# Kernel tuning notes

Hardware: AMD Instinct MI355X
Metric: run time of the kernel (lower is better)

Reference implementation:

```python
import jax, jax.numpy as jnp
import numpy as np

OUT_H, OUT_W = 7, 7
SCALE = 0.25
S = 2  # sample_num per bin axis


def _bilinear(img, y, x):
    """Bilinearly sample img[..., H, W] at float coords (y, x).
    y, x have identical shape G; returns img.shape[:-2] + G.
    Matches RoIAlign CUDA interpolation (zero outside [-1, H]/[-1, W])."""
    H, W = img.shape[-2], img.shape[-1]
    valid = (y > -1.0) & (y < H) & (x > -1.0) & (x < W)
    y = jnp.clip(y, 0.0, H - 1)
    x = jnp.clip(x, 0.0, W - 1)
    y0 = jnp.floor(y).astype(jnp.int32)
    x0 = jnp.floor(x).astype(jnp.int32)
    y1 = jnp.minimum(y0 + 1, H - 1)
    x1 = jnp.minimum(x0 + 1, W - 1)
    ly = y - y0
    lx = x - x0
    hy, hx = 1.0 - ly, 1.0 - lx
    v = (hy * hx * img[..., y0, x0] + hy * lx * img[..., y0, x1]
         + ly * hx * img[..., y1, x0] + ly * lx * img[..., y1, x1])
    return jnp.where(valid, v, 0.0)


def setup_inputs() -> dict:
    key = jax.random.key(0)
    k1, k2, k3, k4, k5 = jax.random.split(key, 5)
    N, C, H, W = 2, 256, 200, 200
    R, MH, MW = 512, 128, 128
    features = jax.random.normal(k1, (N, C, H, W), jnp.float32)
    bidx = jax.random.randint(k2, (R,), 0, N)
    xy1 = jax.random.randint(k3, (R, 2), 0, 672)          # x1, y1 (image coords)
    wh = jax.random.randint(k4, (R, 2), 8, 128)           # box sizes in [8,128)
    xy2 = jnp.minimum(xy1 + wh - 1, 799)                  # x2, y2 inclusive
    rois = jnp.concatenate([bidx[:, None].astype(jnp.float32),
                            xy1.astype(jnp.float32),
                            xy2.astype(jnp.float32)], axis=1)  # [R,5]
    batch_masks = jax.random.uniform(k5, (R, MH, MW), jnp.float32)
    # zero-pad beyond each roi's (h, w), mimicking the list->dense packing
    hv = jnp.arange(MH)[None, :] < (xy2[:, 1] - xy1[:, 1] + 1)[:, None]
    wv = jnp.arange(MW)[None, :] < (xy2[:, 0] - xy1[:, 0] + 1)[:, None]
    batch_masks = batch_masks * (hv[:, :, None] & wv[:, None, :]).astype(jnp.float32)
    return {"features": features, "rois": rois, "batch_masks": batch_masks}


def reference(features, rois, batch_masks):
    """Mask-weighted RoIAlign: per-roi bilinear feature samples are weighted by
    the roi's shape mask (bilinearly sampled in roi-relative image coords),
    then average-pooled over the sub-sample grid of each output bin."""
    C = features.shape[1]

    def one_roi(roi, mask):
        b = roi[0].astype(jnp.int32)
        x1, y1, x2, y2 = roi[1], roi[2], roi[3], roi[4]
        roi_start_w = x1 * SCALE
        roi_start_h = y1 * SCALE
        roi_w = jnp.maximum((x2 - x1 + 1.0) * SCALE, 1.0)
        roi_h = jnp.maximum((y2 - y1 + 1.0) * SCALE, 1.0)
        bin_w = roi_w / OUT_W
        bin_h = roi_h / OUT_H
        # sub-sample offsets: (bin + (i+0.5)/S) for i in [0,S)  -> [OUT*S]
        offs = (jnp.arange(S, dtype=jnp.float32) + 0.5) / S
        ys = roi_start_h + (jnp.arange(OUT_H, dtype=jnp.float32)[:, None] + offs[None, :]).reshape(-1) * bin_h
        xs = roi_start_w + (jnp.arange(OUT_W, dtype=jnp.float32)[:, None] + offs[None, :]).reshape(-1) * bin_w
        yy, xx = jnp.meshgrid(ys, xs, indexing='ij')       # [OUT_H*S, OUT_W*S]
        feat = features[b]                                  # [C, H, W]
        vals = _bilinear(feat, yy, xx)                      # [C, OUT_H*S, OUT_W*S]
        # mask weight at the same sample point, in roi-relative image coords
        my = jnp.clip(yy / SCALE - y1, 0.0, y2 - y1)
        mx = jnp.clip(xx / SCALE - x1, 0.0, x2 - x1)
        wgt = _bilinear(mask, my, mx)                       # [OUT_H*S, OUT_W*S]
        v = (vals * wgt).reshape(C, OUT_H, S, OUT_W, S)
        return v.mean(axis=(2, 4))                          # [C, OUT_H, OUT_W]

    return jax.vmap(one_roi)(rois, batch_masks)             # [R, C, OUT_H, OUT_W]
```

## Files before the change

kernel.cpp:

```cpp
#include <hip/hip_runtime.h>


constexpr int   OUT_H = 7, OUT_W = 7;
constexpr int   NBIN  = OUT_H * OUT_W;
constexpr float SCALE = 0.25f;
constexpr int   S     = 2;
constexpr int   NSAMP = NBIN * S * S;

__global__ __launch_bounds__(256)
void nchw_to_nhwc_kernel(const float* __restrict__ in, float* __restrict__ out,
                         int C, int P) {
    __shared__ float tile[32][33];
    int tx = threadIdx.x;
    int ty = threadIdx.y;
    int gx = blockIdx.x * 32;
    int gy = blockIdx.y * 32;
    int b  = blockIdx.z;

    const float* inb  = in  + (size_t)b * C * P;
    float*       outb = out + (size_t)b * C * P;

#pragma unroll
    for (int j = 0; j < 4; ++j) {
        int cc = gy + ty + 8 * j;
        int p  = gx + tx;
        if (cc < C && p < P)
            tile[ty + 8 * j][tx] = inb[(size_t)cc * P + p];
    }
    __syncthreads();
#pragma unroll
    for (int j = 0; j < 4; ++j) {
        int p  = gx + ty + 8 * j;
        int cc = gy + tx;
        if (cc < C && p < P)
            outb[(size_t)p * C + cc] = tile[tx][ty + 8 * j];
    }
}

__global__ __launch_bounds__(256)
void mask_roialign_nhwc_kernel(const float* __restrict__ nhwc,
                               const float* __restrict__ rois,
                               const float* __restrict__ masks,
                               float*       __restrict__ out,
                               int C, int H, int W, int MH, int MW) {
    __shared__ int   s_off[NSAMP][4];
    __shared__ float s_w[NSAMP][4];
    __shared__ float s_out[256 * NBIN];

    const int r   = blockIdx.x;
    const int tid = threadIdx.x;

    const float* roi = rois + (size_t)r * 5;
    const int   b  = (int)roi[0];
    const float x1 = roi[1], y1 = roi[2], x2 = roi[3], y2 = roi[4];

    if (tid < NSAMP) {
        const int bin = tid >> 2;
        const int sub = tid & 3;
        const int ph  = bin / OUT_W, pw = bin % OUT_W;
        const int iy  = sub >> 1,   ix = sub & 1;

        const float roi_start_w = x1 * SCALE;
        const float roi_start_h = y1 * SCALE;
        const float roi_w = fmaxf((x2 - x1 + 1.0f) * SCALE, 1.0f);
        const float roi_h = fmaxf((y2 - y1 + 1.0f) * SCALE, 1.0f);
        const float bin_w = roi_w / (float)OUT_W;
        const float bin_h = roi_h / (float)OUT_H;

        const float yy = roi_start_h + ((float)ph + ((float)iy + 0.5f) * (1.0f / S)) * bin_h;
        const float xx = roi_start_w + ((float)pw + ((float)ix + 0.5f) * (1.0f / S)) * bin_w;

        const bool valid = (yy > -1.0f) && (yy < (float)H) && (xx > -1.0f) && (xx < (float)W);

        const float* msk = masks + (size_t)r * MH * MW;
        float my = fminf(fmaxf(yy * (1.0f / SCALE) - y1, 0.0f), y2 - y1);
        float mx = fminf(fmaxf(xx * (1.0f / SCALE) - x1, 0.0f), x2 - x1);
        {
            my = fminf(fmaxf(my, 0.0f), (float)(MH - 1));
            mx = fminf(fmaxf(mx, 0.0f), (float)(MW - 1));
        }
        const int my0 = (int)floorf(my), mx0 = (int)floorf(mx);
        const int my1 = min(my0 + 1, MH - 1), mx1 = min(mx0 + 1, MW - 1);
        const float mly = my - (float)my0, mlx = mx - (float)mx0;
        const float mhy = 1.0f - mly,      mhx = 1.0f - mlx;
        const float wgt = mhy * mhx * msk[my0 * MW + mx0] + mhy * mlx * msk[my0 * MW + mx1]
                        + mly * mhx * msk[my1 * MW + mx0] + mly * mlx * msk[my1 * MW + mx1];

        const float yc = fminf(fmaxf(yy, 0.0f), (float)(H - 1));
        const float xc = fminf(fmaxf(xx, 0.0f), (float)(W - 1));
        const int y0  = (int)floorf(yc), x0 = (int)floorf(xc);
        const int y1i = min(y0 + 1, H - 1), x1i = min(x0 + 1, W - 1);
        const float ly = yc - (float)y0, lx = xc - (float)x0;
        const float hy = 1.0f - ly,      hx = 1.0f - lx;

        const float scale_all = (valid ? wgt : 0.0f) * (1.0f / (float)(S * S));
        s_w[tid][0] = hy * hx * scale_all;
        s_w[tid][1] = hy * lx * scale_all;
        s_w[tid][2] = ly * hx * scale_all;
        s_w[tid][3] = ly * lx * scale_all;
        s_off[tid][0] = (y0  * W + x0 ) * C;
        s_off[tid][1] = (y0  * W + x1i) * C;
        s_off[tid][2] = (y1i * W + x0 ) * C;
        s_off[tid][3] = (y1i * W + x1i) * C;
    }
    __syncthreads();

    const int c = tid;
    const float* f = nhwc + (size_t)b * H * W * C + c;

    for (int bin = 0; bin < NBIN; ++bin) {
        float acc = 0.0f;
#pragma unroll
        for (int sub = 0; sub < 4; ++sub) {
            const int s = bin * 4 + sub;
            const int   o0 = s_off[s][0], o1 = s_off[s][1], o2 = s_off[s][2], o3 = s_off[s][3];
            const float w0 = s_w[s][0],   w1 = s_w[s][1],   w2 = s_w[s][2],   w3 = s_w[s][3];
            acc += w0 * f[o0] + w1 * f[o1] + w2 * f[o2] + w3 * f[o3];
        }
        s_out[c * NBIN + bin] = acc;
    }
    __syncthreads();

    float* outr = out + (size_t)r * C * NBIN;
    const float4* s4 = (const float4*)s_out;
    float4*       o4 = (float4*)outr;
    const int nvec = (256 * NBIN) / 4;
    for (int i = tid; i < nvec; i += 256)
        o4[i] = s4[i];
}

__global__ __launch_bounds__(256)
void mask_roialign_kernel(const float* __restrict__ features,
                          const float* __restrict__ rois,
                          const float* __restrict__ masks,
                          float*       __restrict__ out,
                          int C, int H, int W, int MH, int MW) {
    int blk = blockIdx.x;
    int pw  = blk % OUT_W;
    int ph  = (blk / OUT_W) % OUT_H;
    int r   = blk / (OUT_W * OUT_H);
    int c   = threadIdx.x;

    const float* roi = rois + (size_t)r * 5;
    int   b  = (int)roi[0];
    float x1 = roi[1], y1 = roi[2], x2 = roi[3], y2 = roi[4];

    float roi_start_w = x1 * SCALE;
    float roi_start_h = y1 * SCALE;
    float roi_w = fmaxf((x2 - x1 + 1.0f) * SCALE, 1.0f);
    float roi_h = fmaxf((y2 - y1 + 1.0f) * SCALE, 1.0f);
    float bin_w = roi_w / (float)OUT_W;
    float bin_h = roi_h / (float)OUT_H;

    const float* fch = features + ((size_t)b * C + c) * (size_t)(H * W);
    const float* msk = masks + (size_t)r * MH * MW;

    float acc = 0.0f;
#pragma unroll
    for (int iy = 0; iy < S; ++iy) {
        float yy = roi_start_h + ((float)ph + ((float)iy + 0.5f) / (float)S) * bin_h;
#pragma unroll
        for (int ix = 0; ix < S; ++ix) {
            float xx = roi_start_w + ((float)pw + ((float)ix + 0.5f) / (float)S) * bin_w;
            bool valid = (yy > -1.0f) && (yy < (float)H) && (xx > -1.0f) && (xx < (float)W);
            float my = fminf(fmaxf(yy / SCALE - y1, 0.0f), fminf(y2 - y1, (float)(MH - 1)));
            float mx = fminf(fmaxf(xx / SCALE - x1, 0.0f), fminf(x2 - x1, (float)(MW - 1)));
            int my0 = (int)floorf(my), mx0 = (int)floorf(mx);
            int my1 = min(my0 + 1, MH - 1), mx1 = min(mx0 + 1, MW - 1);
            float mly = my - my0, mlx = mx - mx0, mhy = 1.0f - mly, mhx = 1.0f - mlx;
            float wgt = mhy * mhx * msk[my0 * MW + mx0] + mhy * mlx * msk[my0 * MW + mx1]
                      + mly * mhx * msk[my1 * MW + mx0] + mly * mlx * msk[my1 * MW + mx1];
            if (valid) {
                float yc = fminf(fmaxf(yy, 0.0f), (float)(H - 1));
                float xc = fminf(fmaxf(xx, 0.0f), (float)(W - 1));
                int y0 = (int)floorf(yc), x0 = (int)floorf(xc);
                int y1i = min(y0 + 1, H - 1), x1i = min(x0 + 1, W - 1);
                float ly = yc - y0, lx = xc - x0, hy = 1.0f - ly, hx = 1.0f - lx;
                float v = hy * hx * fch[y0  * W + x0 ] + hy * lx * fch[y0  * W + x1i]
                        + ly * hx * fch[y1i * W + x0 ] + ly * lx * fch[y1i * W + x1i];
                acc += wgt * v;
            }
        }
    }
    out[((size_t)r * C + c) * (size_t)NBIN + ph * OUT_W + pw] = acc * (1.0f / (S * S));
}

extern "C" void kernel_launch(void* const* d_in, const int* in_sizes, int n_in,
                              void* d_out, int out_size, void* d_ws, size_t ws_size,
                              hipStream_t stream) {
    const float* features = (const float*)d_in[0];
    const float* rois     = (const float*)d_in[1];
    const float* masks    = (const float*)d_in[2];
    float*       out      = (float*)d_out;

    const int R  = in_sizes[1] / 5;
    const int C  = out_size / (R * NBIN);
    const int H  = 200, W = 200;
    const int MH = 128, MW = 128;
    const int N  = in_sizes[0] / (C * H * W);
    const int P  = H * W;

    const size_t need = (size_t)N * C * P * sizeof(float);
    if (ws_size >= need) {
        float* nhwc = (float*)d_ws;
        dim3 tb(32, 8);
        dim3 tg((P + 31) / 32, (C + 31) / 32, N);
        nchw_to_nhwc_kernel<<<tg, tb, 0, stream>>>(features, nhwc, C, P);

        mask_roialign_nhwc_kernel<<<dim3(R), dim3(256), 0, stream>>>(
            nhwc, rois, masks, out, C, H, W, MH, MW);
    } else {
        mask_roialign_kernel<<<dim3(R * NBIN), dim3(256), 0, stream>>>(
            features, rois, masks, out, C, H, W, MH, MW);
    }
}
```

Measured before the change: 190.6 us.

## Vectorize NHWC transpose with 64x64 tiles and split RoIAlign blocks by channel groups

```diff
diff --git a/kernel.cpp b/kernel.cpp
--- a/kernel.cpp
+++ b/kernel.cpp
@@ -6,34 +6,40 @@
 constexpr float SCALE = 0.25f;
 constexpr int   S     = 2;
 constexpr int   NSAMP = NBIN * S * S;
+constexpr int   CG    = 32;
 
 __global__ __launch_bounds__(256)
-void nchw_to_nhwc_kernel(const float* __restrict__ in, float* __restrict__ out,
-                         int C, int P) {
-    __shared__ float tile[32][33];
-    int tx = threadIdx.x;
-    int ty = threadIdx.y;
-    int gx = blockIdx.x * 32;
-    int gy = blockIdx.y * 32;
-    int b  = blockIdx.z;
+void nchw_to_nhwc_v4_kernel(const float* __restrict__ in, float* __restrict__ out,
+                            int C, int P) {
+    __shared__ float tile[64][65];
+    const int tx = threadIdx.x;
+    const int ty = threadIdx.y;
+    const int gx = blockIdx.x * 64;
+    const int gy = blockIdx.y * 64;
+    const int b  = blockIdx.z;
 
     const float* inb  = in  + (size_t)b * C * P;
     float*       outb = out + (size_t)b * C * P;
 
 #pragma unroll
     for (int j = 0; j < 4; ++j) {
-        int cc = gy + ty + 8 * j;
-        int p  = gx + tx;
-        if (cc < C && p < P)
-            tile[ty + 8 * j][tx] = inb[(size_t)cc * P + p];
+        const int c_local = ty + 16 * j;
+        const float4 v = *(const float4*)&inb[(size_t)(gy + c_local) * P + gx + 4 * tx];
+        tile[c_local][4 * tx + 0] = v.x;
+        tile[c_local][4 * tx + 1] = v.y;
+        tile[c_local][4 * tx + 2] = v.z;
+        tile[c_local][4 * tx + 3] = v.w;
     }
     __syncthreads();
 #pragma unroll
     for (int j = 0; j < 4; ++j) {
-        int p  = gx + ty + 8 * j;
-        int cc = gy + tx;
-        if (cc < C && p < P)
-            outb[(size_t)p * C + cc] = tile[tx][ty + 8 * j];
+        const int p_local = ty + 16 * j;
+        float4 v;
+        v.x = tile[4 * tx + 0][p_local];
+        v.y = tile[4 * tx + 1][p_local];
+        v.z = tile[4 * tx + 2][p_local];
+        v.w = tile[4 * tx + 3][p_local];
+        *(float4*)&outb[(size_t)(gx + p_local) * C + gy + 4 * tx] = v;
     }
 }
 
@@ -45,9 +51,10 @@
                                int C, int H, int W, int MH, int MW) {
     __shared__ int   s_off[NSAMP][4];
     __shared__ float s_w[NSAMP][4];
-    __shared__ float s_out[256 * NBIN];
+    __shared__ float s_out[CG * NBIN];
 
     const int r   = blockIdx.x;
+    const int cg  = blockIdx.y;
     const int tid = threadIdx.x;
 
     const float* roi = rois + (size_t)r * 5;
@@ -75,10 +82,8 @@
         const float* msk = masks + (size_t)r * MH * MW;
         float my = fminf(fmaxf(yy * (1.0f / SCALE) - y1, 0.0f), y2 - y1);
         float mx = fminf(fmaxf(xx * (1.0f / SCALE) - x1, 0.0f), x2 - x1);
-        {
-            my = fminf(fmaxf(my, 0.0f), (float)(MH - 1));
-            mx = fminf(fmaxf(mx, 0.0f), (float)(MW - 1));
-        }
+        my = fminf(fmaxf(my, 0.0f), (float)(MH - 1));
+        mx = fminf(fmaxf(mx, 0.0f), (float)(MW - 1));
         const int my0 = (int)floorf(my), mx0 = (int)floorf(mx);
         const int my1 = min(my0 + 1, MH - 1), mx1 = min(mx0 + 1, MW - 1);
         const float mly = my - (float)my0, mlx = mx - (float)mx0;
@@ -105,10 +110,12 @@
     }
     __syncthreads();
 
-    const int c = tid;
+    const int cl = tid & (CG - 1);
+    const int bg = tid >> 5;
+    const int c  = cg * CG + cl;
     const float* f = nhwc + (size_t)b * H * W * C + c;
 
-    for (int bin = 0; bin < NBIN; ++bin) {
+    for (int bin = bg; bin < NBIN; bin += 8) {
         float acc = 0.0f;
 #pragma unroll
         for (int sub = 0; sub < 4; ++sub) {
@@ -117,15 +124,15 @@
             const float w0 = s_w[s][0],   w1 = s_w[s][1],   w2 = s_w[s][2],   w3 = s_w[s][3];
             acc += w0 * f[o0] + w1 * f[o1] + w2 * f[o2] + w3 * f[o3];
         }
-        s_out[c * NBIN + bin] = acc;
+        s_out[cl * NBIN + bin] = acc;
     }
     __syncthreads();
 
-    float* outr = out + (size_t)r * C * NBIN;
+    float* outr = out + ((size_t)r * C + (size_t)cg * CG) * NBIN;
+    const int ntot = CG * NBIN;
     const float4* s4 = (const float4*)s_out;
     float4*       o4 = (float4*)outr;
-    const int nvec = (256 * NBIN) / 4;
-    for (int i = tid; i < nvec; i += 256)
+    for (int i = tid; i < ntot / 4; i += 256)
         o4[i] = s4[i];
 }
 
@@ -201,13 +208,14 @@
     const int P  = H * W;
 
     const size_t need = (size_t)N * C * P * sizeof(float);
-    if (ws_size >= need) {
+    const bool tiles_ok = (C % 64 == 0) && (P % 64 == 0) && (C % CG == 0);
+    if (ws_size >= need && tiles_ok) {
         float* nhwc = (float*)d_ws;
-        dim3 tb(32, 8);
-        dim3 tg((P + 31) / 32, (C + 31) / 32, N);
-        nchw_to_nhwc_kernel<<<tg, tb, 0, stream>>>(features, nhwc, C, P);
-
-        mask_roialign_nhwc_kernel<<<dim3(R), dim3(256), 0, stream>>>(
+        dim3 tb(16, 16);
+        dim3 tg(P / 64, C / 64, N);
+        nchw_to_nhwc_v4_kernel<<<tg, tb, 0, stream>>>(features, nhwc, C, P);
+
+        mask_roialign_nhwc_kernel<<<dim3(R, C / CG), dim3(256), 0, stream>>>(
             nhwc, rois, masks, out, C, H, W, MH, MW);
     } else {
         mask_roialign_kernel<<<dim3(R * NBIN), dim3(256), 0, stream>>>(
```

After: 182.6 us. -4.2%, faster.
